# Kernel optimization log

Hardware: AMD Instinct MI355X
Metric: run time of the kernel (lower is better)

The kernel has to match this reference:

```python
import jax, jax.numpy as jnp
import numpy as np

D_OUT = 128
PATCH = 16
D_INNER = 256   # 2*d_out (canonical Mamba expand=2)
D_STATE = 16
D_CONV = 4
DT_RANK = 8     # ceil(d_out/16)


def setup_inputs() -> dict:
    key = jax.random.key(0)
    ks = jax.random.split(key, 10)
    f = jnp.float32
    rgb = jax.random.normal(ks[0], (4, 90, 3, 224, 224), f)
    conv_w = jax.random.normal(ks[1], (64, 3, 3, 7, 7), f) * 0.05
    conv_b = jnp.zeros((64,), f)
    bn_gamma = jnp.ones((64,), f)
    bn_beta = jnp.zeros((64,), f)
    bn_mean = jnp.zeros((64,), f)
    bn_var = jnp.ones((64,), f)
    proj_w = jax.random.normal(ks[2], (D_OUT, 64 * 3 * 3), f) * 0.04
    proj_b = jnp.zeros((D_OUT,), f)
    m_in_w = jax.random.normal(ks[3], (2 * D_INNER, D_OUT), f) * 0.05
    m_conv_w = jax.random.normal(ks[4], (D_INNER, 1, D_CONV), f) * 0.2
    m_conv_b = jnp.zeros((D_INNER,), f)
    m_x_w = jax.random.normal(ks[5], (DT_RANK + 2 * D_STATE, D_INNER), f) * 0.05
    m_dt_w = jax.random.normal(ks[6], (D_INNER, DT_RANK), f) * 0.1
    m_dt_b = jnp.full((D_INNER,), -4.0, f)  # softplus -> small dt, stable scan
    m_A_log = jnp.log(jnp.tile(jnp.arange(1, D_STATE + 1, dtype=f), (D_INNER, 1)))
    m_D = jnp.ones((D_INNER,), f)
    m_out_w = jax.random.normal(ks[7], (D_OUT, D_INNER), f) * 0.05
    return dict(rgb=rgb, conv_w=conv_w, conv_b=conv_b, bn_gamma=bn_gamma,
                bn_beta=bn_beta, bn_mean=bn_mean, bn_var=bn_var,
                proj_w=proj_w, proj_b=proj_b, m_in_w=m_in_w, m_conv_w=m_conv_w,
                m_conv_b=m_conv_b, m_x_w=m_x_w, m_dt_w=m_dt_w, m_dt_b=m_dt_b,
                m_A_log=m_A_log, m_D=m_D, m_out_w=m_out_w)


def _adaptive_pool_hw(x, out_h, out_w):
    # x: [b,c,t,h,w] -> [b,c,t,out_h,out_w], PyTorch adaptive_avg_pool bins
    h, w = x.shape[-2], x.shape[-1]
    rows = []
    for i in range(out_h):
        sh, eh = i * h // out_h, -(-(i + 1) * h) // out_h
        cols = []
        for j in range(out_w):
            sw, ew = j * w // out_w, -(-(j + 1) * w) // out_w
            cols.append(x[..., sh:eh, sw:ew].mean(axis=(-2, -1)))
        rows.append(jnp.stack(cols, axis=-1))
    return jnp.stack(rows, axis=-2)


def _mamba(x, in_w, conv_w, conv_b, x_w, dt_w, dt_b, A_log, Dp, out_w):
    b, l, d = x.shape
    xm, res = jnp.split(x @ in_w.T, 2, axis=-1)  # each [b,l,d_inner]
    # depthwise causal conv1d over time
    xc = jnp.transpose(xm, (0, 2, 1))  # [b,d_inner,l]
    xc = jax.lax.conv_general_dilated(
        xc, conv_w, (1,), [(D_CONV - 1, 0)],
        dimension_numbers=('NCH', 'OIH', 'NCH'), feature_group_count=D_INNER)
    xm = jax.nn.silu(jnp.transpose(xc + conv_b[None, :, None], (0, 2, 1)))
    A = -jnp.exp(A_log)  # [d_inner, d_state]
    xdbl = xm @ x_w.T
    dt, Bm, Cm = jnp.split(xdbl, [DT_RANK, DT_RANK + D_STATE], axis=-1)
    delta = jax.nn.softplus(dt @ dt_w.T + dt_b)  # [b,l,d_inner]
    dA = jnp.exp(jnp.einsum('bld,dn->bldn', delta, A))
    dBx = jnp.einsum('bld,bln,bld->bldn', delta, Bm, xm)

    def step(h, inp):
        dA_t, dBx_t, C_t = inp
        h = dA_t * h + dBx_t  # [b,d_inner,d_state]
        return h, jnp.einsum('bdn,bn->bd', h, C_t)

    h0 = jnp.zeros((b, D_INNER, D_STATE), xm.dtype)
    _, ys = jax.lax.scan(step, h0, (jnp.moveaxis(dA, 1, 0),
                                    jnp.moveaxis(dBx, 1, 0),
                                    jnp.moveaxis(Cm, 1, 0)))
    y = jnp.moveaxis(ys, 0, 1) + xm * Dp
    y = y * jax.nn.silu(res)
    return y @ out_w.T


def reference(rgb, conv_w, conv_b, bn_gamma, bn_beta, bn_mean, bn_var,
              proj_w, proj_b, m_in_w, m_conv_w, m_conv_b, m_x_w, m_dt_w,
              m_dt_b, m_A_log, m_D, m_out_w):
    x = jnp.transpose(rgb, (0, 2, 1, 3, 4))  # b c t h w
    x = jax.lax.conv_general_dilated(
        x, conv_w, (1, 4, 4), [(1, 1), (3, 3), (3, 3)],
        dimension_numbers=('NCDHW', 'OIDHW', 'NCDHW'))
    x = x + conv_b[None, :, None, None, None]
    inv = (bn_gamma / jnp.sqrt(bn_var + 1e-5))[None, :, None, None, None]
    x = x * inv + (bn_beta - bn_mean * bn_gamma / jnp.sqrt(bn_var + 1e-5))[None, :, None, None, None]
    x = jax.nn.gelu(x, approximate=False)
    x = _adaptive_pool_hw(x, 56 // PATCH, 56 // PATCH)  # [b,64,t,3,3]
    b, c, t = x.shape[0], x.shape[1], x.shape[2]
    x = jnp.transpose(x, (0, 2, 1, 3, 4)).reshape(b, t, -1)  # b t (c hh ww)
    x = x @ proj_w.T + proj_b
    return _mamba(x, m_in_w, m_conv_w, m_conv_b, m_x_w, m_dt_w, m_dt_b,
                  m_A_log, m_D, m_out_w)
```

## Files before the change

### kernel.cpp

```cpp
#include <hip/hip_runtime.h>
#include <math.h>
#include <stdint.h>

typedef _Float16 half8 __attribute__((ext_vector_type(8)));
typedef _Float16 half4h __attribute__((ext_vector_type(4)));
typedef float f32x4 __attribute__((ext_vector_type(4)));

#define ACOLS 232
#define AROWS 100

__global__ __launch_bounds__(256) void pad_kernel(const float* __restrict__ rgb,
                                                  _Float16* __restrict__ pim)
{
    int idx = blockIdx.x * 256 + threadIdx.x;
    if (idx >= 250608 * 29) return;
    int row = idx / 29, seg = idx - row * 29;
    int ihp = row % 227; int pr = row / 227;
    int c = pr % 3; int btp = pr / 3;
    int tp = btp % 92; int b = btp / 92;
    int t = tp - 1, ih = ihp - 3;
    float v[8];
    #pragma unroll
    for (int j = 0; j < 8; ++j) v[j] = 0.f;
    if ((unsigned)t < 90u && (unsigned)ih < 224u) {
        const float* src = rgb + (((size_t)(b * 90 + t) * 3 + c) * 224 + ih) * 224;
        if (seg >= 1 && seg <= 27) {
            __builtin_memcpy(v, src + seg * 8 - 3, 32);
        } else if (seg == 0) {
            #pragma unroll
            for (int j = 3; j < 8; ++j) v[j] = src[j - 3];
        } else {
            #pragma unroll
            for (int j = 0; j < 3; ++j) v[j] = src[221 + j];
        }
    }
    half8 hv;
    #pragma unroll
    for (int j = 0; j < 8; ++j) hv[j] = (_Float16)v[j];
    *(half8*)(pim + (size_t)row * ACOLS + seg * 8) = hv;
}

__global__ void wprep_kernel(const float* __restrict__ conv_w, _Float16* __restrict__ wBh)
{
    int idx = blockIdx.x * 256 + threadIdx.x;
    if (idx >= 36864) return;
    int rowlog = idx >> 9, rem = idx & 511, co = rem >> 3, kw = rem & 7;
    int p = rowlog >> 3, khs = rowlog & 7;
    int c = p / 3, kt = p - c * 3;
    float v = 0.f;
    if (khs < 7 && kw < 7)
        v = conv_w[(((size_t)(co * 3 + c) * 3 + kt) * 7 + khs) * 7 + kw];
    wBh[idx] = (_Float16)v;
}

static __device__ __forceinline__ half8 ld8(const _Float16* p) {
    half4h lo = *(const half4h*)p;
    half4h hi = *(const half4h*)(p + 4);
    return __builtin_shufflevector(lo, hi, 0, 1, 2, 3, 4, 5, 6, 7);
}

static __device__ __forceinline__ float gelu_exact(float v) {
    float z = __builtin_fabsf(v) * 0.70710678118654752f;
    float t = __builtin_amdgcn_rcpf(__builtin_fmaf(0.3275911f, z, 1.f));
    float p = __builtin_fmaf(1.061405429f, t, -1.453152027f);
    p = __builtin_fmaf(p, t, 1.421413741f);
    p = __builtin_fmaf(p, t, -0.284496736f);
    p = __builtin_fmaf(p, t, 0.254829592f);
    p *= t;
    float e = __expf(-z * z);
    float er = __builtin_fmaf(-p, e, 1.f);
    float se = __builtin_copysignf(er, v);
    return 0.5f * v * (1.f + se);
}

typedef const __attribute__((address_space(1))) uint32_t gu32;
typedef __attribute__((address_space(3))) uint32_t lu32;

__global__ __launch_bounds__(256) void conv_mfma_kernel(
    const _Float16* __restrict__ pim, const _Float16* __restrict__ wBh,
    const float* __restrict__ conv_b, const float* __restrict__ bn_gamma,
    const float* __restrict__ bn_beta, const float* __restrict__ bn_mean,
    const float* __restrict__ bn_var, float* __restrict__ partial)
{
    __shared__ __align__(16) char smem[AROWS * ACOLS * 2];
    _Float16* s_a = (_Float16*)smem;
    float*    s_r = (float*)smem;

    const int bx = blockIdx.x;
    const int bt = blockIdx.y;
    const int b = bt / 90, t = bt % 90;
    const int tid = threadIdx.x;
    const int lane = tid & 63;
    const int wid = __builtin_amdgcn_readfirstlane(tid >> 6);

    for (int cid = wid; cid < 45; cid += 4) {
        int p = cid / 5, j = cid - p * 5;
        int c = p / 3, kt = p - c * 3;
        const char* gsrc = (const char*)(pim +
            ((size_t)((b * 92 + t + kt) * 3 + c) * 227 + 8 * bx) * ACOLS)
            + j * 1024 + lane * 16;
        char* ldst = smem + p * 5104 + j * 1024;
        if (j < 4 || lane < 63)
            __builtin_amdgcn_global_load_lds((gu32*)gsrc, (lu32*)ldst, 16, 0, 0);
    }
    if (tid < 29) {
        half8 z = {};
        *(half8*)(s_a + 99 * ACOLS + tid * 8) = z;
    }
    __syncthreads();

    const int wn = wid & 1, wm = wid >> 1;
    const int l15 = lane & 15, q = lane >> 4;

    f32x4 acc[2][2][2] = {};
    int owA = wm * 32 + l15;  if (owA > 55) owA = 55;
    int owB = owA + 16;       if (owB > 55) owB = 55;
    const int co0 = wn * 32 + l15;
    const int co1 = co0 + 16;
    const _Float16* baseA = s_a + q * ACOLS + 4 * owA;
    const _Float16* baseB = s_a + q * ACOLS + 4 * owB;
    const _Float16* bp0 = wBh + (size_t)q * 512 + co0 * 8;
    const _Float16* bp1 = bp0 + 128;

    float vg0 = bn_gamma[co0], vg1 = bn_gamma[co1];
    float vv0 = bn_var[co0],   vv1 = bn_var[co1];
    float vb0 = bn_beta[co0],  vb1 = bn_beta[co1];
    float vm0 = bn_mean[co0],  vm1 = bn_mean[co1];
    float vc0 = conv_b[co0],   vc1 = conv_b[co1];

    #pragma unroll
    for (int kk = 0; kk < 18; ++kk) {
        const int ro = (4 * kk + 3 * (kk >> 1)) * ACOLS;
        half8 b0 = *(const half8*)(bp0 + (size_t)kk * 2048);
        half8 b1 = *(const half8*)(bp1 + (size_t)kk * 2048);
        half8 a00 = ld8(baseA + ro);
        half8 a01 = ld8(baseB + ro);
        half8 a10 = ld8(baseA + ro + 4 * ACOLS);
        half8 a11 = ld8(baseB + ro + 4 * ACOLS);

        acc[0][0][0] = __builtin_amdgcn_mfma_f32_16x16x32_f16(a00, b0, acc[0][0][0], 0, 0, 0);
        acc[0][0][1] = __builtin_amdgcn_mfma_f32_16x16x32_f16(a00, b1, acc[0][0][1], 0, 0, 0);
        acc[0][1][0] = __builtin_amdgcn_mfma_f32_16x16x32_f16(a01, b0, acc[0][1][0], 0, 0, 0);
        acc[0][1][1] = __builtin_amdgcn_mfma_f32_16x16x32_f16(a01, b1, acc[0][1][1], 0, 0, 0);
        acc[1][0][0] = __builtin_amdgcn_mfma_f32_16x16x32_f16(a10, b0, acc[1][0][0], 0, 0, 0);
        acc[1][0][1] = __builtin_amdgcn_mfma_f32_16x16x32_f16(a10, b1, acc[1][0][1], 0, 0, 0);
        acc[1][1][0] = __builtin_amdgcn_mfma_f32_16x16x32_f16(a11, b0, acc[1][1][0], 0, 0, 0);
        acc[1][1][1] = __builtin_amdgcn_mfma_f32_16x16x32_f16(a11, b1, acc[1][1][1], 0, 0, 0);
    }
    __syncthreads();

    float inv[2], sh[2], cb[2];
    inv[0] = vg0 / sqrtf(vv0 + 1e-5f);
    sh[0]  = vb0 - vm0 * inv[0];
    cb[0]  = vc0;
    inv[1] = vg1 / sqrtf(vv1 + 1e-5f);
    sh[1]  = vb1 - vm1 * inv[1];
    cb[1]  = vc1;
    #pragma unroll
    for (int h = 0; h < 2; ++h) {
        #pragma unroll
        for (int n = 0; n < 2; ++n) {
            float s0 = 0.f, s1 = 0.f, s2 = 0.f;
            #pragma unroll
            for (int i = 0; i < 2; ++i) {
                #pragma unroll
                for (int reg = 0; reg < 4; ++reg) {
                    int m = wm * 32 + i * 16 + q * 4 + reg;
                    float v = (acc[h][i][n][reg] + cb[n]) * inv[n] + sh[n];
                    float g = gelu_exact(v);
                    s0 += (m < 18) ? g : 0.f;
                    s1 += (m >= 18 && m < 37) ? g : 0.f;
                    s2 += (m >= 37 && m < 56) ? g : 0.f;
                }
            }
            int co = n ? co1 : co0;
            float* dst = s_r + (((wm * 4 + q) * 2 + h) * 64 + co) * 3;
            dst[0] = s0; dst[1] = s1; dst[2] = s2;
        }
    }
    __syncthreads();

    if (tid < 192) {
        int co = tid / 3, j = tid % 3;
        #pragma unroll
        for (int h = 0; h < 2; ++h) {
            float s = 0.f;
            #pragma unroll
            for (int wq = 0; wq < 8; ++wq)
                s += s_r[((wq * 2 + h) * 64 + co) * 3 + j];
            partial[((size_t)(bt * 56 + 2 * bx + h) * 64 + co) * 3 + j] = s;
        }
    }
}

__global__ __launch_bounds__(256) void ppi_kernel(
    const float* __restrict__ partial, const float* __restrict__ proj_w,
    const float* __restrict__ proj_b, const float* __restrict__ m_in_w,
    float* __restrict__ xm_raw)
{
    __shared__ __align__(16) float s_part[10752];
    __shared__ __align__(16) float s_pool[576];
    __shared__ __align__(16) float s_xp[128];
    int bt = blockIdx.x, tid = threadIdx.x;

    const f32x4* src4 = (const f32x4*)(partial + (size_t)bt * 10752);
    f32x4* dst4 = (f32x4*)s_part;
    for (int i = tid; i < 2688; i += 256) dst4[i] = src4[i];
    __syncthreads();

    for (int f = tid; f < 576; f += 256) {
        int co = f / 9, r = f % 9, i = r / 3, j = r % 3;
        const int sh[3] = {0, 18, 37}, eh[3] = {18, 37, 56};
        const float cnt[3] = {18.f, 19.f, 19.f};
        float s = 0.f;
        for (int oh = sh[i]; oh < eh[i]; ++oh)
            s += s_part[oh * 192 + co * 3 + j];
        s_pool[f] = s / (cnt[i] * cnt[j]);
    }
    __syncthreads();
    if (tid < 128) {
        const f32x4* w = (const f32x4*)(proj_w + (size_t)tid * 576);
        const f32x4* x4 = (const f32x4*)s_pool;
        f32x4 a = {};
        #pragma unroll 4
        for (int f = 0; f < 144; ++f) a += w[f] * x4[f];
        s_xp[tid] = proj_b[tid] + a.x + a.y + a.z + a.w;
    }
    __syncthreads();
    for (int o = tid; o < 512; o += 256) {
        const f32x4* w = (const f32x4*)(m_in_w + (size_t)o * 128);
        const f32x4* x4 = (const f32x4*)s_xp;
        f32x4 a = {};
        #pragma unroll 4
        for (int f = 0; f < 32; ++f) a += w[f] * x4[f];
        xm_raw[(size_t)bt * 512 + o] = a.x + a.y + a.z + a.w;
    }
}

__global__ __launch_bounds__(256) void dxd_kernel(
    const float* __restrict__ xm_raw, const float* __restrict__ m_conv_w,
    const float* __restrict__ m_conv_b, const float* __restrict__ m_x_w,
    const float* __restrict__ m_dt_w, const float* __restrict__ m_dt_b,
    float* __restrict__ xc, float* __restrict__ xdbl, float* __restrict__ delta)
{
    __shared__ __align__(16) float s_xc[256];
    __shared__ float s_xd[40];
    int bt = blockIdx.x, d = threadIdx.x;
    int b = bt / 90, l = bt % 90;
    float s = m_conv_b[d];
    #pragma unroll
    for (int k = 0; k < 4; ++k) {
        int lk = l - 3 + k;
        if (lk >= 0) s += xm_raw[(size_t)(b * 90 + lk) * 512 + d] * m_conv_w[d * 4 + k];
    }
    float xcv = s / (1.f + expf(-s));
    s_xc[d] = xcv;
    xc[(size_t)bt * 256 + d] = xcv;
    __syncthreads();
    if (d < 40) {
        const f32x4* w = (const f32x4*)(m_x_w + (size_t)d * 256);
        const f32x4* x4 = (const f32x4*)s_xc;
        f32x4 a = {};
        #pragma unroll 4
        for (int f = 0; f < 64; ++f) a += w[f] * x4[f];
        float v = a.x + a.y + a.z + a.w;
        s_xd[d] = v;
        xdbl[(size_t)bt * 40 + d] = v;
    }
    __syncthreads();
    float t2 = m_dt_b[d];
    #pragma unroll
    for (int r = 0; r < 8; ++r) t2 += s_xd[r] * m_dt_w[d * 8 + r];
    delta[(size_t)bt * 256 + d] = (t2 > 20.f) ? t2 : log1pf(expf(t2));
}

__global__ __launch_bounds__(128) void scan_kernel(
    const float* __restrict__ xc, const float* __restrict__ xdbl,
    const float* __restrict__ delta, const float* __restrict__ m_A_log,
    const float* __restrict__ m_D, const float* __restrict__ xm_raw,
    float* __restrict__ y)
{
    int b = blockIdx.x >> 1;
    int d = (blockIdx.x & 1) * 128 + threadIdx.x;
    float A[16], h[16];
    #pragma unroll
    for (int n = 0; n < 16; ++n) { A[n] = -expf(m_A_log[d * 16 + n]); h[n] = 0.f; }
    float Dd = m_D[d];
    size_t base = (size_t)b * 90;
    float dl = delta[base * 256 + d];
    float x  = xc[base * 256 + d];
    float r  = xm_raw[base * 512 + 256 + d];
    for (int l = 0; l < 90; ++l) {
        size_t bt = base + l;
        float dln = 0.f, xn = 0.f, rn = 0.f;
        if (l < 89) {
            dln = delta[(bt + 1) * 256 + d];
            xn  = xc[(bt + 1) * 256 + d];
            rn  = xm_raw[(bt + 1) * 512 + 256 + d];
        }
        const float* Bc = xdbl + bt * 40 + 8;
        float yl = 0.f;
        #pragma unroll
        for (int n = 0; n < 16; ++n) {
            float dA = expf(dl * A[n]);
            h[n] = dA * h[n] + dl * Bc[n] * x;
            yl += h[n] * Bc[16 + n];
        }
        yl += x * Dd;
        float sr = r / (1.f + expf(-r));
        y[bt * 256 + d] = yl * sr;
        dl = dln; x = xn; r = rn;
    }
}

__global__ __launch_bounds__(128) void outproj_kernel(
    const float* __restrict__ y, const float* __restrict__ m_out_w,
    float* __restrict__ out)
{
    __shared__ __align__(16) float s_y[256];
    int bt = blockIdx.x, tid = threadIdx.x;
    for (int i = tid; i < 256; i += 128) s_y[i] = y[(size_t)bt * 256 + i];
    __syncthreads();
    const f32x4* w = (const f32x4*)(m_out_w + (size_t)tid * 256);
    const f32x4* x4 = (const f32x4*)s_y;
    f32x4 a = {};
    #pragma unroll 4
    for (int f = 0; f < 64; ++f) a += w[f] * x4[f];
    out[(size_t)bt * 128 + tid] = a.x + a.y + a.z + a.w;
}

extern "C" void kernel_launch(void* const* d_in, const int* in_sizes, int n_in,
                              void* d_out, int out_size, void* d_ws, size_t ws_size,
                              hipStream_t stream) {
    const float* rgb      = (const float*)d_in[0];
    const float* conv_w   = (const float*)d_in[1];
    const float* conv_b   = (const float*)d_in[2];
    const float* bn_gamma = (const float*)d_in[3];
    const float* bn_beta  = (const float*)d_in[4];
    const float* bn_mean  = (const float*)d_in[5];
    const float* bn_var   = (const float*)d_in[6];
    const float* proj_w   = (const float*)d_in[7];
    const float* proj_b   = (const float*)d_in[8];
    const float* m_in_w   = (const float*)d_in[9];
    const float* m_conv_w = (const float*)d_in[10];
    const float* m_conv_b = (const float*)d_in[11];
    const float* m_x_w    = (const float*)d_in[12];
    const float* m_dt_w   = (const float*)d_in[13];
    const float* m_dt_b   = (const float*)d_in[14];
    const float* m_A_log  = (const float*)d_in[15];
    const float* m_D      = (const float*)d_in[16];
    const float* m_out_w  = (const float*)d_in[17];
    float* out = (float*)d_out;

    float* ws      = (float*)d_ws;
    float* partial = ws;
    float* xm_raw  = partial + 3870720;
    float* xc      = xm_raw + 184320;
    float* xdbl    = xc + 92160;
    float* delta   = xdbl + 14400;
    float* yb      = delta + 92160;
    _Float16* wBh  = (_Float16*)(yb + 92160);
    _Float16* pim  = (_Float16*)(yb + 92160 + 18432);

    pad_kernel<<<28390, 256, 0, stream>>>(rgb, pim);
    wprep_kernel<<<144, 256, 0, stream>>>(conv_w, wBh);
    conv_mfma_kernel<<<dim3(28, 360), 256, 0, stream>>>(pim, wBh, conv_b, bn_gamma,
                                                        bn_beta, bn_mean, bn_var, partial);
    ppi_kernel<<<360, 256, 0, stream>>>(partial, proj_w, proj_b, m_in_w, xm_raw);
    dxd_kernel<<<360, 256, 0, stream>>>(xm_raw, m_conv_w, m_conv_b, m_x_w,
                                        m_dt_w, m_dt_b, xc, xdbl, delta);
    scan_kernel<<<8, 128, 0, stream>>>(xc, xdbl, delta, m_A_log, m_D, xm_raw, yb);
    outproj_kernel<<<360, 128, 0, stream>>>(yb, m_out_w, out);
}
```

Baseline: 631.3 us.

## Pipeline conv input staging with per-plane async loads overlapping MFMA

The conv kernel used to load all nine input planes into LDS and wait at one barrier before any MFMA work. Now it issues three planes up front and, in each of nine phases, waits on vmcnt for the plane it needs, hits a barrier, issues the load three planes ahead, then runs that plane's two K-steps at raised wave priority. This overlaps global-to-LDS transfer with matrix math inside each block. The cost is many more barriers and hand-tuned vmcnt counts that depend on each wave's load count, which could give wrong results if they are off.

```diff
diff --git a/kernel.cpp b/kernel.cpp
--- a/kernel.cpp
+++ b/kernel.cpp
@@ -93,21 +93,29 @@
     const int lane = tid & 63;
     const int wid = __builtin_amdgcn_readfirstlane(tid >> 6);
 
-    for (int cid = wid; cid < 45; cid += 4) {
-        int p = cid / 5, j = cid - p * 5;
-        int c = p / 3, kt = p - c * 3;
-        const char* gsrc = (const char*)(pim +
-            ((size_t)((b * 92 + t + kt) * 3 + c) * 227 + 8 * bx) * ACOLS)
-            + j * 1024 + lane * 16;
-        char* ldst = smem + p * 5104 + j * 1024;
-        if (j < 4 || lane < 63)
-            __builtin_amdgcn_global_load_lds((gu32*)gsrc, (lu32*)ldst, 16, 0, 0);
-    }
+    auto stage = [&](int p) {
+        int c_ = p / 3, kt_ = p - c_ * 3;
+        const char* gp = (const char*)(pim +
+            ((size_t)((b * 92 + t + kt_) * 3 + c_) * 227 + 8 * bx) * ACOLS);
+        char* lp = smem + p * 5104;
+        if (wid < 3) {
+            __builtin_amdgcn_global_load_lds((gu32*)(gp + wid * 1024 + lane * 16),
+                                             (lu32*)(lp + wid * 1024), 16, 0, 0);
+        } else {
+            __builtin_amdgcn_global_load_lds((gu32*)(gp + 3072 + lane * 16),
+                                             (lu32*)(lp + 3072), 16, 0, 0);
+            if (lane < 63)
+                __builtin_amdgcn_global_load_lds((gu32*)(gp + 4096 + lane * 16),
+                                                 (lu32*)(lp + 4096), 16, 0, 0);
+        }
+    };
+
+    stage(0); stage(1); stage(2);
     if (tid < 29) {
         half8 z = {};
         *(half8*)(s_a + 99 * ACOLS + tid * 8) = z;
     }
-    __syncthreads();
+    asm volatile("s_waitcnt lgkmcnt(0)" ::: "memory");
 
     const int wn = wid & 1, wm = wid >> 1;
     const int l15 = lane & 15, q = lane >> 4;
@@ -122,31 +130,59 @@
     const _Float16* bp0 = wBh + (size_t)q * 512 + co0 * 8;
     const _Float16* bp1 = bp0 + 128;
 
+#define KK(kkc) do { \
+    const int ro = (4 * (kkc) + 3 * ((kkc) >> 1)) * ACOLS; \
+    half8 b0 = *(const half8*)(bp0 + (size_t)(kkc) * 2048); \
+    half8 b1 = *(const half8*)(bp1 + (size_t)(kkc) * 2048); \
+    half8 a00 = ld8(baseA + ro); \
+    half8 a01 = ld8(baseB + ro); \
+    half8 a10 = ld8(baseA + ro + 4 * ACOLS); \
+    half8 a11 = ld8(baseB + ro + 4 * ACOLS); \
+    acc[0][0][0] = __builtin_amdgcn_mfma_f32_16x16x32_f16(a00, b0, acc[0][0][0], 0, 0, 0); \
+    acc[0][0][1] = __builtin_amdgcn_mfma_f32_16x16x32_f16(a00, b1, acc[0][0][1], 0, 0, 0); \
+    acc[0][1][0] = __builtin_amdgcn_mfma_f32_16x16x32_f16(a01, b0, acc[0][1][0], 0, 0, 0); \
+    acc[0][1][1] = __builtin_amdgcn_mfma_f32_16x16x32_f16(a01, b1, acc[0][1][1], 0, 0, 0); \
+    acc[1][0][0] = __builtin_amdgcn_mfma_f32_16x16x32_f16(a10, b0, acc[1][0][0], 0, 0, 0); \
+    acc[1][0][1] = __builtin_amdgcn_mfma_f32_16x16x32_f16(a10, b1, acc[1][0][1], 0, 0, 0); \
+    acc[1][1][0] = __builtin_amdgcn_mfma_f32_16x16x32_f16(a11, b0, acc[1][1][0], 0, 0, 0); \
+    acc[1][1][1] = __builtin_amdgcn_mfma_f32_16x16x32_f16(a11, b1, acc[1][1][1], 0, 0, 0); \
+} while (0)
+
+#define WAITV(n1, n3) do { \
+    if (wid == 3) asm volatile("s_waitcnt vmcnt(" #n3 ")" ::: "memory"); \
+    else          asm volatile("s_waitcnt vmcnt(" #n1 ")" ::: "memory"); \
+} while (0)
+
+#define PHASE(p, W) do { \
+    W; \
+    __builtin_amdgcn_s_barrier(); \
+    if ((p) + 3 <= 8) stage((p) + 3); \
+    __builtin_amdgcn_s_setprio(1); \
+    KK(2 * (p)); \
+    KK(2 * (p) + 1); \
+    __builtin_amdgcn_s_setprio(0); \
+} while (0)
+
+    PHASE(0, WAITV(1, 2));
+    PHASE(1, WAITV(1, 2));
+    PHASE(2, WAITV(1, 2));
+    PHASE(3, WAITV(1, 2));
+    PHASE(4, WAITV(1, 2));
+    PHASE(5, WAITV(1, 2));
+    PHASE(6, WAITV(1, 2));
+    PHASE(7, WAITV(0, 0));
+    PHASE(8, WAITV(0, 0));
+
+#undef PHASE
+#undef WAITV
+#undef KK
+
     float vg0 = bn_gamma[co0], vg1 = bn_gamma[co1];
     float vv0 = bn_var[co0],   vv1 = bn_var[co1];
     float vb0 = bn_beta[co0],  vb1 = bn_beta[co1];
     float vm0 = bn_mean[co0],  vm1 = bn_mean[co1];
     float vc0 = conv_b[co0],   vc1 = conv_b[co1];
 
-    #pragma unroll
-    for (int kk = 0; kk < 18; ++kk) {
-        const int ro = (4 * kk + 3 * (kk >> 1)) * ACOLS;
-        half8 b0 = *(const half8*)(bp0 + (size_t)kk * 2048);
-        half8 b1 = *(const half8*)(bp1 + (size_t)kk * 2048);
-        half8 a00 = ld8(baseA + ro);
-        half8 a01 = ld8(baseB + ro);
-        half8 a10 = ld8(baseA + ro + 4 * ACOLS);
-        half8 a11 = ld8(baseB + ro + 4 * ACOLS);
-
-        acc[0][0][0] = __builtin_amdgcn_mfma_f32_16x16x32_f16(a00, b0, acc[0][0][0], 0, 0, 0);
-        acc[0][0][1] = __builtin_amdgcn_mfma_f32_16x16x32_f16(a00, b1, acc[0][0][1], 0, 0, 0);
-        acc[0][1][0] = __builtin_amdgcn_mfma_f32_16x16x32_f16(a01, b0, acc[0][1][0], 0, 0, 0);
-        acc[0][1][1] = __builtin_amdgcn_mfma_f32_16x16x32_f16(a01, b1, acc[0][1][1], 0, 0, 0);
-        acc[1][0][0] = __builtin_amdgcn_mfma_f32_16x16x32_f16(a10, b0, acc[1][0][0], 0, 0, 0);
-        acc[1][0][1] = __builtin_amdgcn_mfma_f32_16x16x32_f16(a10, b1, acc[1][0][1], 0, 0, 0);
-        acc[1][1][0] = __builtin_amdgcn_mfma_f32_16x16x32_f16(a11, b0, acc[1][1][0], 0, 0, 0);
-        acc[1][1][1] = __builtin_amdgcn_mfma_f32_16x16x32_f16(a11, b1, acc[1][1][1], 0, 0, 0);
-    }
     __syncthreads();
 
     float inv[2], sh[2], cb[2];
@@ -183,12 +219,12 @@
     if (tid < 192) {
         int co = tid / 3, j = tid % 3;
         #pragma unroll
-        for (int h = 0; h < 2; ++h) {
+        for (int hh = 0; hh < 2; ++hh) {
             float s = 0.f;
             #pragma unroll
             for (int wq = 0; wq < 8; ++wq)
-                s += s_r[((wq * 2 + h) * 64 + co) * 3 + j];
-            partial[((size_t)(bt * 56 + 2 * bx + h) * 64 + co) * 3 + j] = s;
+                s += s_r[((wq * 2 + hh) * 64 + co) * 3 + j];
+            partial[((size_t)(bt * 56 + 2 * bx + hh) * 64 + co) * 3 + j] = s;
         }
     }
 }
```

Result: no change. 641.9 us (+1.7%).

## Compute one output row per conv block with per-plane LDS tiles

Applied to the files above, without the earlier changes.

The conv MFMA kernel now computes one output row per block instead of two. The grid doubles along x, and each block loads only the 7 input rows per (channel, kt) plane into LDS. This roughly halves LDS use and the accumulator registers per block, which should raise occupancy and remove the padding-row fill. The cost is that the overlapping input rows between adjacent output rows are no longer reused within a block, so global-to-LDS traffic grows and twice as many blocks must be launched.

```diff
diff --git a/kernel.cpp b/kernel.cpp
--- a/kernel.cpp
+++ b/kernel.cpp
@@ -7,7 +7,6 @@
 typedef float f32x4 __attribute__((ext_vector_type(4)));
 
 #define ACOLS 232
-#define AROWS 100
 
 __global__ __launch_bounds__(256) void pad_kernel(const float* __restrict__ rgb,
                                                   _Float16* __restrict__ pim)
@@ -82,7 +81,7 @@
     const float* __restrict__ bn_beta, const float* __restrict__ bn_mean,
     const float* __restrict__ bn_var, float* __restrict__ partial)
 {
-    __shared__ __align__(16) char smem[AROWS * ACOLS * 2];
+    __shared__ __align__(16) char smem[9 * 3248];
     _Float16* s_a = (_Float16*)smem;
     float*    s_r = (float*)smem;
 
@@ -93,32 +92,31 @@
     const int lane = tid & 63;
     const int wid = __builtin_amdgcn_readfirstlane(tid >> 6);
 
-    for (int cid = wid; cid < 45; cid += 4) {
-        int p = cid / 5, j = cid - p * 5;
-        int c = p / 3, kt = p - c * 3;
-        const char* gsrc = (const char*)(pim +
-            ((size_t)((b * 92 + t + kt) * 3 + c) * 227 + 8 * bx) * ACOLS)
-            + j * 1024 + lane * 16;
-        char* ldst = smem + p * 5104 + j * 1024;
-        if (j < 4 || lane < 63)
-            __builtin_amdgcn_global_load_lds((gu32*)gsrc, (lu32*)ldst, 16, 0, 0);
-    }
-    if (tid < 29) {
-        half8 z = {};
-        *(half8*)(s_a + 99 * ACOLS + tid * 8) = z;
-    }
-    __syncthreads();
+    for (int p = wid; p < 9; p += 4) {
+        int c_ = p / 3, kt_ = p - c_ * 3;
+        const char* gp = (const char*)(pim +
+            ((size_t)((b * 92 + t + kt_) * 3 + c_) * 227 + 4 * bx) * ACOLS);
+        char* lp = smem + p * 3248;
+        __builtin_amdgcn_global_load_lds((gu32*)(gp + lane * 16),        (lu32*)(lp),        16, 0, 0);
+        __builtin_amdgcn_global_load_lds((gu32*)(gp + 1024 + lane * 16), (lu32*)(lp + 1024), 16, 0, 0);
+        __builtin_amdgcn_global_load_lds((gu32*)(gp + 2048 + lane * 16), (lu32*)(lp + 2048), 16, 0, 0);
+        if (lane < 11)
+            __builtin_amdgcn_global_load_lds((gu32*)(gp + 3072 + lane * 16), (lu32*)(lp + 3072), 16, 0, 0);
+    }
 
     const int wn = wid & 1, wm = wid >> 1;
     const int l15 = lane & 15, q = lane >> 4;
 
-    f32x4 acc[2][2][2] = {};
+    f32x4 acc[2][2] = {};
     int owA = wm * 32 + l15;  if (owA > 55) owA = 55;
     int owB = owA + 16;       if (owB > 55) owB = 55;
     const int co0 = wn * 32 + l15;
     const int co1 = co0 + 16;
-    const _Float16* baseA = s_a + q * ACOLS + 4 * owA;
-    const _Float16* baseB = s_a + q * ACOLS + 4 * owB;
+    const int khsOdd = (q == 3) ? 6 : (4 + q);
+    const _Float16* baseEA = s_a + q * ACOLS + 4 * owA;
+    const _Float16* baseEB = s_a + q * ACOLS + 4 * owB;
+    const _Float16* baseOA = s_a + khsOdd * ACOLS + 4 * owA;
+    const _Float16* baseOB = s_a + khsOdd * ACOLS + 4 * owB;
     const _Float16* bp0 = wBh + (size_t)q * 512 + co0 * 8;
     const _Float16* bp1 = bp0 + 128;
 
@@ -128,24 +126,22 @@
     float vm0 = bn_mean[co0],  vm1 = bn_mean[co1];
     float vc0 = conv_b[co0],   vc1 = conv_b[co1];
 
+    __syncthreads();
+
     #pragma unroll
     for (int kk = 0; kk < 18; ++kk) {
-        const int ro = (4 * kk + 3 * (kk >> 1)) * ACOLS;
+        const int ro = (kk >> 1) * 1624;
+        const _Float16* bA = (kk & 1) ? baseOA : baseEA;
+        const _Float16* bB = (kk & 1) ? baseOB : baseEB;
         half8 b0 = *(const half8*)(bp0 + (size_t)kk * 2048);
         half8 b1 = *(const half8*)(bp1 + (size_t)kk * 2048);
-        half8 a00 = ld8(baseA + ro);
-        half8 a01 = ld8(baseB + ro);
-        half8 a10 = ld8(baseA + ro + 4 * ACOLS);
-        half8 a11 = ld8(baseB + ro + 4 * ACOLS);
-
-        acc[0][0][0] = __builtin_amdgcn_mfma_f32_16x16x32_f16(a00, b0, acc[0][0][0], 0, 0, 0);
-        acc[0][0][1] = __builtin_amdgcn_mfma_f32_16x16x32_f16(a00, b1, acc[0][0][1], 0, 0, 0);
-        acc[0][1][0] = __builtin_amdgcn_mfma_f32_16x16x32_f16(a01, b0, acc[0][1][0], 0, 0, 0);
-        acc[0][1][1] = __builtin_amdgcn_mfma_f32_16x16x32_f16(a01, b1, acc[0][1][1], 0, 0, 0);
-        acc[1][0][0] = __builtin_amdgcn_mfma_f32_16x16x32_f16(a10, b0, acc[1][0][0], 0, 0, 0);
-        acc[1][0][1] = __builtin_amdgcn_mfma_f32_16x16x32_f16(a10, b1, acc[1][0][1], 0, 0, 0);
-        acc[1][1][0] = __builtin_amdgcn_mfma_f32_16x16x32_f16(a11, b0, acc[1][1][0], 0, 0, 0);
-        acc[1][1][1] = __builtin_amdgcn_mfma_f32_16x16x32_f16(a11, b1, acc[1][1][1], 0, 0, 0);
+        half8 a0 = ld8(bA + ro);
+        half8 a1 = ld8(bB + ro);
+
+        acc[0][0] = __builtin_amdgcn_mfma_f32_16x16x32_f16(a0, b0, acc[0][0], 0, 0, 0);
+        acc[0][1] = __builtin_amdgcn_mfma_f32_16x16x32_f16(a0, b1, acc[0][1], 0, 0, 0);
+        acc[1][0] = __builtin_amdgcn_mfma_f32_16x16x32_f16(a1, b0, acc[1][0], 0, 0, 0);
+        acc[1][1] = __builtin_amdgcn_mfma_f32_16x16x32_f16(a1, b1, acc[1][1], 0, 0, 0);
     }
     __syncthreads();
 
@@ -157,39 +153,33 @@
     sh[1]  = vb1 - vm1 * inv[1];
     cb[1]  = vc1;
     #pragma unroll
-    for (int h = 0; h < 2; ++h) {
+    for (int n = 0; n < 2; ++n) {
+        float s0 = 0.f, s1 = 0.f, s2 = 0.f;
         #pragma unroll
-        for (int n = 0; n < 2; ++n) {
-            float s0 = 0.f, s1 = 0.f, s2 = 0.f;
+        for (int i = 0; i < 2; ++i) {
             #pragma unroll
-            for (int i = 0; i < 2; ++i) {
-                #pragma unroll
-                for (int reg = 0; reg < 4; ++reg) {
-                    int m = wm * 32 + i * 16 + q * 4 + reg;
-                    float v = (acc[h][i][n][reg] + cb[n]) * inv[n] + sh[n];
-                    float g = gelu_exact(v);
-                    s0 += (m < 18) ? g : 0.f;
-                    s1 += (m >= 18 && m < 37) ? g : 0.f;
-                    s2 += (m >= 37 && m < 56) ? g : 0.f;
-                }
+            for (int reg = 0; reg < 4; ++reg) {
+                int m = wm * 32 + i * 16 + q * 4 + reg;
+                float v = (acc[i][n][reg] + cb[n]) * inv[n] + sh[n];
+                float g = gelu_exact(v);
+                s0 += (m < 18) ? g : 0.f;
+                s1 += (m >= 18 && m < 37) ? g : 0.f;
+                s2 += (m >= 37 && m < 56) ? g : 0.f;
             }
-            int co = n ? co1 : co0;
-            float* dst = s_r + (((wm * 4 + q) * 2 + h) * 64 + co) * 3;
-            dst[0] = s0; dst[1] = s1; dst[2] = s2;
         }
+        int co = n ? co1 : co0;
+        float* dst = s_r + ((wm * 4 + q) * 64 + co) * 3;
+        dst[0] = s0; dst[1] = s1; dst[2] = s2;
     }
     __syncthreads();
 
     if (tid < 192) {
         int co = tid / 3, j = tid % 3;
+        float s = 0.f;
         #pragma unroll
-        for (int h = 0; h < 2; ++h) {
-            float s = 0.f;
-            #pragma unroll
-            for (int wq = 0; wq < 8; ++wq)
-                s += s_r[((wq * 2 + h) * 64 + co) * 3 + j];
-            partial[((size_t)(bt * 56 + 2 * bx + h) * 64 + co) * 3 + j] = s;
-        }
+        for (int wq = 0; wq < 8; ++wq)
+            s += s_r[(wq * 64 + co) * 3 + j];
+        partial[((size_t)(bt * 56 + bx) * 64 + co) * 3 + j] = s;
     }
 }
 
@@ -364,7 +354,7 @@
 
     pad_kernel<<<28390, 256, 0, stream>>>(rgb, pim);
     wprep_kernel<<<144, 256, 0, stream>>>(conv_w, wBh);
-    conv_mfma_kernel<<<dim3(28, 360), 256, 0, stream>>>(pim, wBh, conv_b, bn_gamma,
+    conv_mfma_kernel<<<dim3(56, 360), 256, 0, stream>>>(pim, wBh, conv_b, bn_gamma,
                                                         bn_beta, bn_mean, bn_var, partial);
     ppi_kernel<<<360, 256, 0, stream>>>(partial, proj_w, proj_b, m_in_w, xm_raw);
     dxd_kernel<<<360, 256, 0, stream>>>(xm_raw, m_conv_w, m_conv_b, m_x_w,
```

Measured after the change: 666.1 us. +5.5%, slower.
